# Performance work log

Hardware: AMD Instinct MI355X
Metric: run time of the kernel (lower is better)

## Reference

```python
import jax, jax.numpy as jnp
import numpy as np

B, T, D, H = 8, 2048, 1024, 16
HD = D // H          # head_dim = 64
SC = H               # scales = n_heads = 16
DECAY_MIN, DECAY_MAX = 0.3, 0.99


def setup_inputs() -> dict:
    key = jax.random.key(0)
    k_x, k_in, k_mix, k_gw, k_gb, k_out = jax.random.split(key, 6)
    x = jax.random.normal(k_x, (B, T, D), dtype=jnp.float32)
    pad_mask = jnp.zeros((B, T), dtype=bool)  # True = PAD
    inv = 1.0 / np.sqrt(D)
    W_in = jax.random.uniform(k_in, (D, D), jnp.float32, -inv, inv)
    W_out = jax.random.uniform(k_out, (D, D), jnp.float32, -inv, inv)
    W_gate = jax.random.uniform(k_gw, (D, D), jnp.float32, -inv, inv)
    b_gate = jax.random.uniform(k_gb, (D,), jnp.float32, -inv, inv)
    state_mix = jax.random.normal(k_mix, (H, SC, HD), jnp.float32) / np.sqrt(HD)
    p = jnp.linspace(DECAY_MIN, DECAY_MAX, SC)
    logit_decay = jnp.tile(jnp.log(p / (1.0 - p))[None, :], (H, 1))  # [H, SC]
    return {"x": x, "pad_mask": pad_mask, "W_in": W_in, "state_mix": state_mix,
            "logit_decay": logit_decay, "W_gate": W_gate, "b_gate": b_gate,
            "W_out": W_out}


def reference(x, pad_mask, W_in, state_mix, logit_decay, W_gate, b_gate, W_out):
    Bc, Tc, Dc = x.shape
    Hc, Sc, Hd = state_mix.shape
    h = (x @ W_in.T).reshape(Bc, Tc, Hc, Hd)          # [B,T,H,Hd]
    decays = jax.nn.sigmoid(logit_decay)              # [H,SC]
    keep = 1.0 - pad_mask.astype(x.dtype)             # [B,T], 1 where not PAD

    def step(S, inp):
        ht, mt = inp                                  # [B,H,Hd], [B]
        S = (decays[None, :, :, None] * S + ht[:, :, None, :]) \
            * mt[:, None, None, None]                 # [B,H,SC,Hd]
        read = jnp.einsum('bhsd,hsd->bhd', S, state_mix)
        return S, read

    S0 = jnp.zeros((Bc, Hc, Sc, Hd), dtype=x.dtype)
    _, reads = jax.lax.scan(step, S0, (h.transpose(1, 0, 2, 3), keep.T))
    y = reads.transpose(1, 0, 2, 3).reshape(Bc, Tc, Dc)
    g = jax.nn.sigmoid(x @ W_gate.T + b_gate)
    y = g * y + (1.0 - g) * x
    return y @ W_out.T
```

## Files before the change

### kernel.cpp

```cpp
#include <hip/hip_runtime.h>

#define B_  8
#define T_  2048
#define D_  1024
#define H_  16
#define HD_ 64
#define SC_ 16
#define NC_ 32
#define CT_ 64

typedef __attribute__((ext_vector_type(8))) short short8;
typedef __attribute__((ext_vector_type(4))) float f32x4;

__device__ inline unsigned short f2bf(float f) {
  union { float f; unsigned u; } v; v.f = f;
  unsigned r = v.u + 0x7FFFu + ((v.u >> 16) & 1u);
  return (unsigned short)(r >> 16);
}
__device__ inline float bf2f(unsigned short b) {
  union { unsigned u; float f; } v; v.u = ((unsigned)b) << 16; return v.f;
}

__device__ inline void gl_lds16(const unsigned short* g, unsigned short* l) {
  __builtin_amdgcn_global_load_lds(
      (const __attribute__((address_space(1))) unsigned int*)(g),
      (__attribute__((address_space(3))) unsigned int*)(l), 16, 0, 0);
}

__global__ void conv_f32_bf16(const float* __restrict__ in,
                              unsigned short* __restrict__ out, int n4) {
  int i = blockIdx.x * 256 + threadIdx.x;
  if (i >= n4) return;
  float4 v = ((const float4*)in)[i];
  ushort4 o;
  o.x = f2bf(v.x); o.y = f2bf(v.y); o.z = f2bf(v.z); o.w = f2bf(v.w);
  ((ushort4*)out)[i] = o;
}

template<int MODE>
__global__ __launch_bounds__(256, 2)
void gemm_bt(const unsigned short* __restrict__ A,
             const unsigned short* __restrict__ Bt,
             void* __restrict__ C1, void* __restrict__ C2,
             const float* __restrict__ bgate,
             int M, int N, int K) {
  __shared__ unsigned short As[128 * 64];
  __shared__ unsigned short Bs[128 * 64];
  const int tid  = threadIdx.x;
  const int lane = tid & 63;
  const int w    = tid >> 6;
  const int wm   = w >> 1, wn = w & 1;
  const int l15  = lane & 15, l4 = lane >> 4;
  const int srow   = lane >> 3;
  const int schunk = (lane & 7) ^ srow;
  const int nbn  = N >> 7;
  const int nwg  = gridDim.x;
  int bid = blockIdx.x;
  int b2 = ((nwg & 7) == 0) ? ((bid & 7) * (nwg >> 3) + (bid >> 3)) : bid;
  const int bm = (b2 / nbn) << 7;
  const int bn = (b2 % nbn) << 7;

  f32x4 acc[4][4] = {};

  for (int k0 = 0; k0 < K; k0 += 64) {
#pragma unroll
    for (int i = 0; i < 4; ++i) {
      int q = (w << 2) + i;
      int r = (q << 3) + srow;
      gl_lds16(A  + (size_t)(bm + r) * K + k0 + (schunk << 3), As + (q << 9));
      gl_lds16(Bt + (size_t)(bn + r) * K + k0 + (schunk << 3), Bs + (q << 9));
    }
    __syncthreads();
#pragma unroll
    for (int ks = 0; ks < 2; ++ks) {
      short8 af[4], bf[4];
#pragma unroll
      for (int i = 0; i < 4; ++i) {
        int ra = (wm << 6) + (i << 4) + l15;
        int kc = (ks << 2) + l4;
        af[i] = *(const short8*)(&As[ra * 64 + ((kc ^ (ra & 7)) << 3)]);
        int rb = (wn << 6) + (i << 4) + l15;
        bf[i] = *(const short8*)(&Bs[rb * 64 + ((kc ^ (rb & 7)) << 3)]);
      }
#pragma unroll
      for (int mi = 0; mi < 4; ++mi)
#pragma unroll
        for (int ni = 0; ni < 4; ++ni)
          acc[mi][ni] = __builtin_amdgcn_mfma_f32_16x16x32_bf16(
              af[mi], bf[ni], acc[mi][ni], 0, 0, 0);
    }
    __syncthreads();
  }

  const int rbase = bm + (wm << 6) + (l4 << 2);
  const bool is_gate = (MODE == 2) && (bn >= 1024);
  void* dst = is_gate ? C2 : C1;
  const int cb = is_gate ? (bn - 1024) : bn;
  const int cbase = cb + (wn << 6) + l15;
  const int CN = (MODE == 2) ? 1024 : N;
  float bgv[4];
  if (is_gate) {
#pragma unroll
    for (int ni = 0; ni < 4; ++ni) bgv[ni] = bgate[cbase + (ni << 4)];
  }
#pragma unroll
  for (int mi = 0; mi < 4; ++mi)
#pragma unroll
    for (int ni = 0; ni < 4; ++ni)
#pragma unroll
      for (int r = 0; r < 4; ++r) {
        size_t row = rbase + (mi << 4) + r;
        int col = cbase + (ni << 4);
        if (MODE == 0) {
          ((float*)dst)[row * CN + col] = acc[mi][ni][r];
        } else if (is_gate) {
          float g = 1.f / (1.f + __expf(-(acc[mi][ni][r] + bgv[ni])));
          ((unsigned short*)dst)[row * CN + col] = f2bf(g);
        } else {
          ((unsigned short*)dst)[row * CN + col] = f2bf(acc[mi][ni][r]);
        }
      }
}

__device__ inline bool chunk_has_pad(const unsigned char* pp) {
  const unsigned long long* p8 = (const unsigned long long*)pp;
  unsigned long long v = 0;
#pragma unroll
  for (int i = 0; i < CT_ / 8; ++i) v |= p8[i];
  return v != 0ull;
}

__global__ void scan_pass1(const unsigned short* __restrict__ hb,
                           const unsigned char* __restrict__ pad,
                           const float* __restrict__ ldec,
                           float* __restrict__ Schunk,
                           float* __restrict__ akeep) {
  int gid = blockIdx.x * 256 + threadIdx.x;
  int d  = gid & 63;
  int hh = (gid >> 6) & 15;
  int c  = (gid >> 10) & (NC_ - 1);
  int b  = gid >> 15;
  float dec[SC_], S[SC_];
#pragma unroll
  for (int s = 0; s < SC_; ++s) {
    dec[s] = 1.f / (1.f + __expf(-ldec[hh * SC_ + s]));
    S[s] = 0.f;
  }
  const int t0 = c * CT_;
  const unsigned short* hp = hb + (size_t)(b * T_ + t0) * D_ + hh * HD_ + d;
  const unsigned char* pp = pad + b * T_ + t0;
  bool anypad = chunk_has_pad(pp);
  if (!anypad) {
    for (int t = 0; t < CT_; ++t) {
      float ht = bf2f(*hp); hp += D_;
#pragma unroll
      for (int s = 0; s < SC_; ++s) S[s] = dec[s] * S[s] + ht;
    }
  } else {
    for (int t = 0; t < CT_; ++t) {
      float ht = bf2f(*hp); hp += D_;
      float k = pp[t] ? 0.f : 1.f;
#pragma unroll
      for (int s = 0; s < SC_; ++s) S[s] = (dec[s] * S[s] + ht) * k;
    }
  }
  size_t base = ((size_t)((b * NC_ + c) * H_ + hh) * SC_) * HD_ + d;
#pragma unroll
  for (int s = 0; s < SC_; ++s) Schunk[base + s * HD_] = S[s];
  if (hh == 0 && d == 0) akeep[b * NC_ + c] = anypad ? 0.f : 1.f;
}

__global__ void scan_combine(float* __restrict__ Schunk,
                             const float* __restrict__ akeep,
                             const float* __restrict__ ldec) {
  int gid = blockIdx.x * 256 + threadIdx.x;
  int d  = gid & 63;
  int s  = (gid >> 6) & 15;
  int hh = (gid >> 10) & 15;
  int b  = gid >> 14;
  float dec  = 1.f / (1.f + __expf(-ldec[hh * SC_ + s]));
  float dpow = __powf(dec, (float)CT_);
  float carry = 0.f;
  for (int c = 0; c < NC_; ++c) {
    size_t idx = ((size_t)((b * NC_ + c) * H_ + hh) * SC_ + s) * HD_ + d;
    float e = Schunk[idx];
    Schunk[idx] = carry;
    float Ac = (akeep[b * NC_ + c] != 0.f) ? dpow : 0.f;
    carry = Ac * carry + e;
  }
}

__global__ void scan_pass2(const unsigned short* __restrict__ hb,
                           const unsigned char* __restrict__ pad,
                           const float* __restrict__ ldec,
                           const float* __restrict__ mix,
                           const float* __restrict__ Sstart,
                           const unsigned short* __restrict__ gb,
                           unsigned short* __restrict__ xy) {
  int gid = blockIdx.x * 256 + threadIdx.x;
  int d  = gid & 63;
  int hh = (gid >> 6) & 15;
  int c  = (gid >> 10) & (NC_ - 1);
  int b  = gid >> 15;
  float dec[SC_], mx[SC_], S[SC_];
  size_t sbase = ((size_t)((b * NC_ + c) * H_ + hh) * SC_) * HD_ + d;
#pragma unroll
  for (int s = 0; s < SC_; ++s) {
    dec[s] = 1.f / (1.f + __expf(-ldec[hh * SC_ + s]));
    mx[s]  = mix[(hh * SC_ + s) * HD_ + d];
    S[s]   = Sstart[sbase + s * HD_];
  }
  const int t0 = c * CT_;
  const int col = hh * HD_ + d;
  size_t off = (size_t)(b * T_ + t0) * D_ + col;
  const unsigned char* pp = pad + b * T_ + t0;
  bool anypad = chunk_has_pad(pp);
  if (!anypad) {
    for (int t = 0; t < CT_; ++t, off += D_) {
      float ht = bf2f(hb[off]);
      float rd = 0.f;
#pragma unroll
      for (int s = 0; s < SC_; ++s) {
        S[s] = dec[s] * S[s] + ht;
        rd  += mx[s] * S[s];
      }
      float g  = bf2f(gb[off]);
      float xv = bf2f(xy[off]);
      xy[off] = f2bf(fmaf(g, rd - xv, xv));
    }
  } else {
    for (int t = 0; t < CT_; ++t, off += D_) {
      float ht = bf2f(hb[off]);
      float k = pp[t] ? 0.f : 1.f;
      float rd = 0.f;
#pragma unroll
      for (int s = 0; s < SC_; ++s) {
        S[s] = (dec[s] * S[s] + ht) * k;
        rd  += mx[s] * S[s];
      }
      float g  = bf2f(gb[off]);
      float xv = bf2f(xy[off]);
      xy[off] = f2bf(fmaf(g, rd - xv, xv));
    }
  }
}

extern "C" void kernel_launch(void* const* d_in, const int* in_sizes, int n_in,
                              void* d_out, int out_size, void* d_ws, size_t ws_size,
                              hipStream_t stream) {
  const float* x          = (const float*)d_in[0];
  const unsigned char* pm = (const unsigned char*)d_in[1];
  const float* W_in       = (const float*)d_in[2];
  const float* smix       = (const float*)d_in[3];
  const float* ldec       = (const float*)d_in[4];
  const float* W_gate     = (const float*)d_in[5];
  const float* b_gate     = (const float*)d_in[6];
  const float* W_out      = (const float*)d_in[7];
  float* out = (float*)d_out;
  char* ws = (char*)d_ws;

  const int NX = B_ * T_ * D_;
  const int NW = D_ * D_;

  unsigned short* xb    = (unsigned short*)(ws);
  unsigned short* wbin  = (unsigned short*)(ws + 33554432);
  unsigned short* wbgt  = (unsigned short*)(ws + 35651584);
  unsigned short* wbout = (unsigned short*)(ws + 37748736);
  unsigned short* hb    = (unsigned short*)(ws + 39845888);
  float* Schunk         = (float*)(ws + 73400320);
  float* akeep          = (float*)(ws + 90177536);
  unsigned short* gb    = (unsigned short*)d_out;

  conv_f32_bf16<<<NX / 1024, 256, 0, stream>>>(x, xb, NX / 4);
  conv_f32_bf16<<<NW / 1024, 256, 0, stream>>>(W_in,   wbin,  NW / 4);
  conv_f32_bf16<<<NW / 1024, 256, 0, stream>>>(W_gate, wbgt,  NW / 4);
  conv_f32_bf16<<<NW / 1024, 256, 0, stream>>>(W_out,  wbout, NW / 4);

  const int M = B_ * T_;

  dim3 gg2((M / 128) * (2048 / 128));
  gemm_bt<2><<<gg2, 256, 0, stream>>>(xb, wbin, hb, gb, b_gate, M, 2048, D_);

  dim3 sg1(B_ * NC_ * H_ * HD_ / 256);
  dim3 sgc(B_ * H_ * SC_ * HD_ / 256);
  scan_pass1 <<<sg1, 256, 0, stream>>>(hb, pm, ldec, Schunk, akeep);
  scan_combine<<<sgc, 256, 0, stream>>>(Schunk, akeep, ldec);
  scan_pass2 <<<sg1, 256, 0, stream>>>(hb, pm, ldec, smix, Schunk, gb, xb);

  dim3 gg((M / 128) * (D_ / 128));
  gemm_bt<0><<<gg, 256, 0, stream>>>(xb, wbout, out, nullptr, nullptr, M, D_, D_);
}
```

Before: 197.2 us.

## Halve scan chunk length, merge weight conversions, split read accumulators

Doubles the number of scan chunks (NC 32→64, CT 64→32), giving twice as many threads in the chunked scan passes with shorter serial loops per thread. The three weight fp32→bf16 conversions are merged into a single launch. The 16-term read reduction in pass 2 is split across four independent accumulators to shorten the dependency chain. Schunk moves into the unused upper half of the output buffer, since it now needs twice the space. The combine pass does more sequential carry steps, and Schunk traffic doubles.

```diff
diff --git a/kernel.cpp b/kernel.cpp
--- a/kernel.cpp
+++ b/kernel.cpp
@@ -6,8 +6,8 @@
 #define H_  16
 #define HD_ 64
 #define SC_ 16
-#define NC_ 32
-#define CT_ 64
+#define NC_ 64
+#define CT_ 32
 
 typedef __attribute__((ext_vector_type(8))) short short8;
 typedef __attribute__((ext_vector_type(4))) float f32x4;
@@ -31,6 +31,21 @@
                               unsigned short* __restrict__ out, int n4) {
   int i = blockIdx.x * 256 + threadIdx.x;
   if (i >= n4) return;
+  float4 v = ((const float4*)in)[i];
+  ushort4 o;
+  o.x = f2bf(v.x); o.y = f2bf(v.y); o.z = f2bf(v.z); o.w = f2bf(v.w);
+  ((ushort4*)out)[i] = o;
+}
+
+__global__ void conv_w3(const float* __restrict__ w0, unsigned short* __restrict__ o0,
+                        const float* __restrict__ w1, unsigned short* __restrict__ o1,
+                        const float* __restrict__ w2, unsigned short* __restrict__ o2) {
+  int bid = blockIdx.x;
+  const float* in; unsigned short* out;
+  if (bid < 1024)      { in = w0; out = o0; }
+  else if (bid < 2048) { in = w1; out = o1; bid -= 1024; }
+  else                 { in = w2; out = o2; bid -= 2048; }
+  int i = bid * 256 + threadIdx.x;
   float4 v = ((const float4*)in)[i];
   ushort4 o;
   o.x = f2bf(v.x); o.y = f2bf(v.y); o.z = f2bf(v.z); o.w = f2bf(v.w);
@@ -139,7 +154,7 @@
   int d  = gid & 63;
   int hh = (gid >> 6) & 15;
   int c  = (gid >> 10) & (NC_ - 1);
-  int b  = gid >> 15;
+  int b  = gid >> 16;
   float dec[SC_], S[SC_];
 #pragma unroll
   for (int s = 0; s < SC_; ++s) {
@@ -201,7 +216,7 @@
   int d  = gid & 63;
   int hh = (gid >> 6) & 15;
   int c  = (gid >> 10) & (NC_ - 1);
-  int b  = gid >> 15;
+  int b  = gid >> 16;
   float dec[SC_], mx[SC_], S[SC_];
   size_t sbase = ((size_t)((b * NC_ + c) * H_ + hh) * SC_) * HD_ + d;
 #pragma unroll
@@ -218,12 +233,15 @@
   if (!anypad) {
     for (int t = 0; t < CT_; ++t, off += D_) {
       float ht = bf2f(hb[off]);
-      float rd = 0.f;
-#pragma unroll
-      for (int s = 0; s < SC_; ++s) {
-        S[s] = dec[s] * S[s] + ht;
-        rd  += mx[s] * S[s];
+      float r0 = 0.f, r1 = 0.f, r2 = 0.f, r3 = 0.f;
+#pragma unroll
+      for (int j = 0; j < 4; ++j) {
+        S[j]      = dec[j]      * S[j]      + ht; r0 = fmaf(mx[j],      S[j],      r0);
+        S[j + 4]  = dec[j + 4]  * S[j + 4]  + ht; r1 = fmaf(mx[j + 4],  S[j + 4],  r1);
+        S[j + 8]  = dec[j + 8]  * S[j + 8]  + ht; r2 = fmaf(mx[j + 8],  S[j + 8],  r2);
+        S[j + 12] = dec[j + 12] * S[j + 12] + ht; r3 = fmaf(mx[j + 12], S[j + 12], r3);
       }
+      float rd = (r0 + r1) + (r2 + r3);
       float g  = bf2f(gb[off]);
       float xv = bf2f(xy[off]);
       xy[off] = f2bf(fmaf(g, rd - xv, xv));
@@ -232,12 +250,15 @@
     for (int t = 0; t < CT_; ++t, off += D_) {
       float ht = bf2f(hb[off]);
       float k = pp[t] ? 0.f : 1.f;
-      float rd = 0.f;
-#pragma unroll
-      for (int s = 0; s < SC_; ++s) {
-        S[s] = (dec[s] * S[s] + ht) * k;
-        rd  += mx[s] * S[s];
+      float r0 = 0.f, r1 = 0.f, r2 = 0.f, r3 = 0.f;
+#pragma unroll
+      for (int j = 0; j < 4; ++j) {
+        S[j]      = (dec[j]      * S[j]      + ht) * k; r0 = fmaf(mx[j],      S[j],      r0);
+        S[j + 4]  = (dec[j + 4]  * S[j + 4]  + ht) * k; r1 = fmaf(mx[j + 4],  S[j + 4],  r1);
+        S[j + 8]  = (dec[j + 8]  * S[j + 8]  + ht) * k; r2 = fmaf(mx[j + 8],  S[j + 8],  r2);
+        S[j + 12] = (dec[j + 12] * S[j + 12] + ht) * k; r3 = fmaf(mx[j + 12], S[j + 12], r3);
       }
+      float rd = (r0 + r1) + (r2 + r3);
       float g  = bf2f(gb[off]);
       float xv = bf2f(xy[off]);
       xy[off] = f2bf(fmaf(g, rd - xv, xv));
@@ -260,21 +281,18 @@
   char* ws = (char*)d_ws;
 
   const int NX = B_ * T_ * D_;
-  const int NW = D_ * D_;
 
   unsigned short* xb    = (unsigned short*)(ws);
   unsigned short* wbin  = (unsigned short*)(ws + 33554432);
   unsigned short* wbgt  = (unsigned short*)(ws + 35651584);
   unsigned short* wbout = (unsigned short*)(ws + 37748736);
   unsigned short* hb    = (unsigned short*)(ws + 39845888);
-  float* Schunk         = (float*)(ws + 73400320);
-  float* akeep          = (float*)(ws + 90177536);
+  float* akeep          = (float*)(ws + 73400320);
   unsigned short* gb    = (unsigned short*)d_out;
+  float* Schunk         = (float*)((char*)d_out + 33554432);
 
   conv_f32_bf16<<<NX / 1024, 256, 0, stream>>>(x, xb, NX / 4);
-  conv_f32_bf16<<<NW / 1024, 256, 0, stream>>>(W_in,   wbin,  NW / 4);
-  conv_f32_bf16<<<NW / 1024, 256, 0, stream>>>(W_gate, wbgt,  NW / 4);
-  conv_f32_bf16<<<NW / 1024, 256, 0, stream>>>(W_out,  wbout, NW / 4);
+  conv_w3<<<3072, 256, 0, stream>>>(W_in, wbin, W_gate, wbgt, W_out, wbout);
 
   const int M = B_ * T_;
 
```

Measured after the change: 197.6 us. No clear change (+0.2%).
